# Performance work log

Measured on AMD Instinct MI355X. Metric: run time of the kernel, lower is better.

The kernel has to match this reference:

```python
import jax, jax.numpy as jnp
import numpy as np

B, T, C, H, N = 2, 1024, 2048, 32, 64  # batch, seq, n_embd==dim_att, heads, head_size
EPS_GN = 64e-5  # torch GroupNorm eps=0.00064


def setup_inputs() -> dict:
    key = jax.random.key(0)
    ks = jax.random.split(key, 40)
    def rn(i, shape, s):
        return jax.random.normal(ks[i], shape, dtype=jnp.float32) * s
    return {
        'x': jax.random.normal(ks[0], (B, T, C), dtype=jnp.float32),
        'shift_state': jnp.zeros((B, C), jnp.float32),
        'wkv_state': jnp.zeros((B, H, N, N), jnp.float32),
        'time_maa_x': rn(1, (1, 1, C), 0.3),
        'time_maa_rg': rn(2, (1, 1, C), 0.3),
        'time_maa_wa': rn(3, (1, 1, C), 0.3),
        'time_maa_k': rn(4, (1, 1, C), 0.3),
        'time_maa_v': rn(5, (1, 1, C), 0.3),
        'time_maa_w1': rn(6, (C, 128), 0.02),   # D_MIX_LORA*4 = 128
        'time_maa_w2': rn(7, (4, 32, C), 0.02),
        'time_decay': rn(8, (1, 1, C), 0.5) - 4.0,
        'time_decay_w1': rn(9, (C, 64), 0.02),
        'time_decay_w2': rn(10, (64, C), 0.02),
        'time_faaaa': rn(11, (1, 1, H, N), 0.02),
        'time_aaaaa': rn(12, (1, 1, C), 0.02),
        'time_aaa_w1': rn(13, (C, 16), 0.02),
        'time_aaa_w2': rn(14, (16, C), 0.02),
        'time_kkk_w1': rn(15, (C, 16), 0.02),
        'time_kkk_w2': rn(16, (16, C), 0.02),
        'gate_w1': rn(17, (C, 128), 0.02),
        'gate_w2': rn(18, (128, C), 0.02),
        'ma_w1': rn(19, (C, 16), 0.02),
        'ma_w2': rn(20, (16, C), 0.02),
        'time_misc_a': rn(21, (1, 1, C), 0.02),
        'mk_w1': rn(22, (C, 16), 0.02),
        'mk_w2': rn(23, (16, C), 0.02),
        'time_misc_k': rn(24, (1, 1, C), 0.02),
        'Wr': rn(25, (C, C), 0.5 / np.sqrt(C)),
        'Wk': rn(26, (C, C), 0.05 / np.sqrt(C)),
        'Wv': rn(27, (C, C), 0.5 / np.sqrt(C)),
        'Wo': rn(28, (C, C), 0.5 / np.sqrt(C)),
        'ln_w': jnp.ones((C,), jnp.float32),
        'ln_b': jnp.zeros((C,), jnp.float32),
    }


def _forward(x, shift_state, wkv_state, time_maa_x, time_maa_rg, time_maa_wa,
             time_maa_k, time_maa_v, time_maa_w1, time_maa_w2, time_decay,
             time_decay_w1, time_decay_w2, time_faaaa, time_aaaaa, time_aaa_w1,
             time_aaa_w2, time_kkk_w1, time_kkk_w2, gate_w1, gate_w2, ma_w1,
             ma_w2, time_misc_a, mk_w1, mk_w2, time_misc_k, Wr, Wk, Wv, Wo,
             ln_w, ln_b):
    # token shift difference
    xx = jnp.concatenate([shift_state[:, None, :], x[:, :-1]], axis=1) - x
    xmx = x + xx * time_maa_x
    m = jnp.tanh(xmx @ time_maa_w1).reshape(B, T, 4, -1)   # [B,T,4,32]
    m = jnp.einsum('btfd,fdc->fbtc', m, time_maa_w2)       # [4,B,T,C]
    mrg, mwa, mkm, mv = m[0], m[1], m[2], m[3]
    xrg = x + xx * (time_maa_rg + mrg)
    xwa = x + xx * (time_maa_wa + mwa)
    xk = x + xx * (time_maa_k + mkm)
    xv = x + xx * (time_maa_v + mv)
    r = xrg @ Wr.T
    w = -jax.nn.softplus(-(time_decay + jnp.tanh(xwa @ time_decay_w1) @ time_decay_w2)) - 0.5
    k = xk @ Wk.T
    v = xv @ Wv.T
    g = jnp.tanh(xrg @ gate_w1) @ gate_w2
    kk = k + jnp.tanh(xk @ time_kkk_w1) @ time_kkk_w2
    kkh = kk.reshape(B, T, H, N)
    nrm = jnp.maximum(jnp.linalg.norm(kkh, axis=-1, keepdims=True), 1e-12)  # F.normalize
    kk = (kkh / nrm).reshape(B, T, C)
    a = jax.nn.sigmoid(time_aaaaa + xwa @ time_aaa_w1 @ time_aaa_w2)
    ma = jax.nn.sigmoid(time_misc_a + xwa @ ma_w1 @ ma_w2)
    k = k * ma + k * a * (1.0 - ma)
    mk = jax.nn.sigmoid(time_misc_k + xk @ mk_w1 @ mk_w2)
    k = k * jnp.exp(jnp.minimum(w * mk, 0.0))  # clamp(w*mk, max=0).exp()

    # RWKV-7 recurrence (fused_recurrent_rwkv7 with a=-kk, b=kk*a_gate):
    #   S_t = diag(exp(w_t)) S_{t-1} + b_t (a_t^T S_{t-1}) + k_t v_t^T,  o_t = S_t^T r_t
    def heads(t):
        return jnp.moveaxis(t.reshape(B, T, H, N), 1, 0)  # [T,B,H,N]
    rs, ksq, vs, ws = heads(r), heads(k), heads(v), heads(w)
    a_s, b_s = heads(-kk), heads(kk * a)

    def step(S, inputs):  # S: [B,H,N_key,N_val]
        r_t, k_t, v_t, w_t, a_t, b_t = inputs
        sa = jnp.einsum('bhk,bhkv->bhv', a_t, S)
        S = S * jnp.exp(w_t)[..., None] + k_t[..., None] * v_t[..., None, :] + b_t[..., None] * sa[..., None, :]
        o = jnp.einsum('bhk,bhkv->bhv', r_t, S)
        return S, o

    S_final, o = jax.lax.scan(step, wkv_state, (rs, ksq, vs, ws, a_s, b_s))
    out = jnp.moveaxis(o, 0, 1).reshape(B, T, C)

    # GroupNorm(n_head groups, eps=64e-5), biased variance per head
    y = out.reshape(B * T, H, N)
    mu = y.mean(-1, keepdims=True)
    var = ((y - mu) ** 2).mean(-1, keepdims=True)
    y = (y - mu) / jnp.sqrt(var + EPS_GN)
    y = y * ln_w.reshape(H, N) + ln_b.reshape(H, N)
    xo = y.reshape(B, T, C)

    rh = r.reshape(B, T, H, N)
    kh = k.reshape(B, T, H, N)
    vh = v.reshape(B, T, H, N)
    xo = xo + ((rh * kh * time_faaaa).sum(-1, keepdims=True) * vh).reshape(B, T, C)
    xo = (xo * g) @ Wo.T
    return xo, x[:, -1], S_final


def reference(x, shift_state, wkv_state, time_maa_x, time_maa_rg, time_maa_wa,
              time_maa_k, time_maa_v, time_maa_w1, time_maa_w2, time_decay,
              time_decay_w1, time_decay_w2, time_faaaa, time_aaaaa, time_aaa_w1,
              time_aaa_w2, time_kkk_w1, time_kkk_w2, gate_w1, gate_w2, ma_w1,
              ma_w2, time_misc_a, mk_w1, mk_w2, time_misc_k, Wr, Wk, Wv, Wo,
              ln_w, ln_b):
    return _forward(x, shift_state, wkv_state, time_maa_x, time_maa_rg, time_maa_wa,
                    time_maa_k, time_maa_v, time_maa_w1, time_maa_w2, time_decay,
                    time_decay_w1, time_decay_w2, time_faaaa, time_aaaaa, time_aaa_w1,
                    time_aaa_w2, time_kkk_w1, time_kkk_w2, gate_w1, gate_w2, ma_w1,
                    ma_w2, time_misc_a, mk_w1, mk_w2, time_misc_k, Wr, Wk, Wv, Wo,
                    ln_w, ln_b)
```

## Files before the change

kernel.cpp:

```cpp
#include <hip/hip_runtime.h>
#include <hip/hip_bf16.h>
#include <math.h>


#define B_ 2
#define T_ 1024
#define C_ 2048
#define H_ 32
#define BT_ (B_*T_)
#define BTC_ ((size_t)BT_*C_)
#define CC_ ((size_t)C_*C_)
#define KS_ 8

typedef __bf16 bf16x8 __attribute__((ext_vector_type(8)));
typedef float f32x4 __attribute__((ext_vector_type(4)));

__device__ __forceinline__ float wave64_sum(float v){
#pragma unroll
  for (int d = 1; d < 64; d <<= 1) v += __shfl_xor(v, d, 64);
  return v;
}

__device__ __forceinline__ float dpp_add_xor1(float x){
  int j = __builtin_amdgcn_mov_dpp(__float_as_int(x), 0xB1, 0xF, 0xF, true);
  return x + __int_as_float(j);
}
__device__ __forceinline__ float dpp_add_xor2(float x){
  int j = __builtin_amdgcn_mov_dpp(__float_as_int(x), 0x4E, 0xF, 0xF, true);
  return x + __int_as_float(j);
}
__device__ __forceinline__ float dpp_add_hmir(float x){
  int j = __builtin_amdgcn_mov_dpp(__float_as_int(x), 0x141, 0xF, 0xF, true);
  return x + __int_as_float(j);
}
__device__ __forceinline__ float dpp_add_mir(float x){
  int j = __builtin_amdgcn_mov_dpp(__float_as_int(x), 0x140, 0xF, 0xF, true);
  return x + __int_as_float(j);
}

__device__ __forceinline__ float red16(float x){
  x = dpp_add_xor1(x);
  x = dpp_add_xor2(x);
  x = dpp_add_hmir(x);
  x = dpp_add_mir(x);
  return x;
}

__device__ __forceinline__ size_t bhtn_idx(int r, int c){
  return (((size_t)(r >> 10)*H_ + (c >> 6))*T_ + (r & 1023))*64 + (c & 63);
}

__device__ __forceinline__ void gload_lds16b(const __hip_bfloat16* g, __bf16* l){
  __builtin_amdgcn_global_load_lds((const __attribute__((address_space(1))) void*)g,
                                   (__attribute__((address_space(3))) void*)l, 16, 0, 0);
}

__global__ __launch_bounds__(256) void f2bf_kernel(const float* __restrict__ in,
                                                   __hip_bfloat16* __restrict__ out, size_t n){
  size_t i = (size_t)blockIdx.x*256 + threadIdx.x;
  if (i < n) out[i] = __float2bfloat16(in[i]);
}

__global__ __launch_bounds__(256) void f2bf3_kernel(const float* __restrict__ i0, const float* __restrict__ i1,
                                                    const float* __restrict__ i2,
                                                    __hip_bfloat16* __restrict__ o0, __hip_bfloat16* __restrict__ o1,
                                                    __hip_bfloat16* __restrict__ o2){
  const int z = blockIdx.y;
  const float* in = (z == 0) ? i0 : (z == 1) ? i1 : i2;
  __hip_bfloat16* out = (z == 0) ? o0 : (z == 1) ? o1 : o2;
  size_t i = (size_t)blockIdx.x*256 + threadIdx.x;
  if (i < CC_) out[i] = __float2bfloat16(in[i]);
}

__global__ __launch_bounds__(256) void shift_kernel(const float* __restrict__ x,
                                                    const float* __restrict__ shift,
                                                    const float* __restrict__ maa_x,
                                                    float* __restrict__ xx, __hip_bfloat16* __restrict__ xmx_h,
                                                    float* __restrict__ out1){
  size_t idx = (size_t)blockIdx.x*256 + threadIdx.x;
  int c = (int)(idx % C_);
  size_t bt = idx / C_;
  int t = (int)(bt % T_);
  int b = (int)(bt / T_);
  float xv = x[idx];
  float prev = (t == 0) ? shift[(size_t)b*C_ + c] : x[idx - C_];
  float d = prev - xv;
  xx[idx] = d;
  xmx_h[idx] = __float2bfloat16(xv + d * maa_x[c]);
  if (t == T_-1) out1[(size_t)b*C_ + c] = xv;
}

__global__ __launch_bounds__(256) void tp_pack7(
    const float* __restrict__ w0, const float* __restrict__ w1, const float* __restrict__ w2,
    const float* __restrict__ w3, const float* __restrict__ w4, const float* __restrict__ w5,
    const float* __restrict__ w6, __hip_bfloat16* __restrict__ WtB)
{
  __shared__ float tile[32][33];
  int y = blockIdx.y;
  const float* in; int Nsrc, row_off, panel, yb;
  if      (y < 4)  { in = w0; Nsrc = 128; row_off = 0;  panel = 0; yb = y; }
  else if (y < 6)  { in = w1; Nsrc = 64;  row_off = 0;  panel = 1; yb = y - 4; }
  else if (y < 7)  { in = w2; Nsrc = 16;  row_off = 64; panel = 1; yb = 0; }
  else if (y < 8)  { in = w3; Nsrc = 16;  row_off = 80; panel = 1; yb = 0; }
  else if (y < 12) { in = w4; Nsrc = 128; row_off = 0;  panel = 2; yb = y - 8; }
  else if (y < 13) { in = w5; Nsrc = 16;  row_off = 0;  panel = 3; yb = 0; }
  else             { in = w6; Nsrc = 16;  row_off = 16; panel = 3; yb = 0; }
  __hip_bfloat16* out = WtB + (size_t)panel*128*2048;
  const int t = threadIdx.x;
  const int k0 = blockIdx.x*32, n0 = yb*32;
  const int tn = t & 31, tk = t >> 5;
#pragma unroll
  for (int q = 0; q < 4; q++){
    int ki = tk + 8*q;
    float v = (n0 + tn < Nsrc) ? in[(size_t)(k0+ki)*Nsrc + n0 + tn] : 0.f;
    tile[tn][ki] = v;
  }
  __syncthreads();
#pragma unroll
  for (int q = 0; q < 4; q++){
    int no = tk + 8*q;
    if (n0 + no < Nsrc)
      out[(size_t)(row_off + n0 + no)*2048 + k0 + tn] = __float2bfloat16(tile[no][tn]);
  }
}

__global__ __launch_bounds__(256) void gemm_sk(const __hip_bfloat16* __restrict__ Ah,
                                               const __hip_bfloat16* __restrict__ Bh,
                                               float* __restrict__ parts, int K, int KC){
  __shared__ __bf16 As[2][128*32];
  __shared__ __bf16 Bs[2][128*32];
  const int tid = threadIdx.x;
  const int bm = blockIdx.x*128;
  const int z = blockIdx.y;
  const int wid = tid >> 6, lane = tid & 63;
  const int wr = (wid >> 1)*64, wc = (wid & 1)*64;
  const int fr = lane & 15, kg = lane >> 4;
  const int srow = tid >> 2, sk = (tid & 3)*8;
  f32x4 acc[4][4] = {};
  const int kend = z*KC + KC;
#define SK_STAGE(kt_, b_) do{ \
    gload_lds16b(Ah + (size_t)(bm+srow)*K + (kt_) + sk,    As[b_] + wid*512); \
    gload_lds16b(Ah + (size_t)(bm+srow+64)*K + (kt_) + sk, As[b_] + wid*512 + 64*32); \
    gload_lds16b(Bh + (size_t)(srow)*K + (kt_) + sk,       Bs[b_] + wid*512); \
    gload_lds16b(Bh + (size_t)(srow+64)*K + (kt_) + sk,    Bs[b_] + wid*512 + 64*32); \
  }while(0)
  SK_STAGE(z*KC, 0);
  __builtin_amdgcn_s_waitcnt(0x3F70);
  __builtin_amdgcn_s_barrier();
  __builtin_amdgcn_sched_barrier(0);
  int buf = 0;
  for (int kt = z*KC; kt < kend; kt += 32){
    if (kt + 32 < kend) SK_STAGE(kt+32, buf^1);
    bf16x8 af[4], bfr[4];
#pragma unroll
    for (int i = 0; i < 4; i++){
      af[i]  = *(const bf16x8*)(As[buf] + (wr + i*16 + fr)*32 + kg*8);
      bfr[i] = *(const bf16x8*)(Bs[buf] + (wc + i*16 + fr)*32 + kg*8);
    }
#pragma unroll
    for (int mi = 0; mi < 4; mi++)
#pragma unroll
      for (int ni = 0; ni < 4; ni++)
        acc[mi][ni] = __builtin_amdgcn_mfma_f32_16x16x32_bf16(af[mi], bfr[ni], acc[mi][ni], 0, 0, 0);
    __builtin_amdgcn_sched_barrier(0);
    __builtin_amdgcn_s_waitcnt(0x3F70);
    __builtin_amdgcn_s_barrier();
    __builtin_amdgcn_sched_barrier(0);
    buf ^= 1;
  }
#undef SK_STAGE
  float* Cc = parts + (size_t)z*BT_*128;
  const int orow0 = bm + wr + kg*4;
  const int ocol0 = wc + fr;
#pragma unroll
  for (int mi = 0; mi < 4; mi++)
#pragma unroll
    for (int ni = 0; ni < 4; ni++)
#pragma unroll
      for (int j = 0; j < 4; j++)
        Cc[(size_t)(orow0 + mi*16 + j)*128 + ocol0 + ni*16] = acc[mi][ni][j];
}

__global__ __launch_bounds__(256) void gemm_sk3(
    const __hip_bfloat16* __restrict__ A0, const __hip_bfloat16* __restrict__ A1,
    const __hip_bfloat16* __restrict__ A2,
    const __hip_bfloat16* __restrict__ B0, const __hip_bfloat16* __restrict__ B1,
    const __hip_bfloat16* __restrict__ B2,
    float* __restrict__ P0, float* __restrict__ P1, float* __restrict__ P2, int K, int KC)
{
  __shared__ __bf16 As[2][128*32];
  __shared__ __bf16 Bs[2][128*32];
  const int zi = blockIdx.z;
  const __hip_bfloat16* Ah = (zi == 0) ? A0 : (zi == 1) ? A1 : A2;
  const __hip_bfloat16* Bh = (zi == 0) ? B0 : (zi == 1) ? B1 : B2;
  float* parts = (zi == 0) ? P0 : (zi == 1) ? P1 : P2;
  const int tid = threadIdx.x;
  const int bm = blockIdx.x*128;
  const int z = blockIdx.y;
  const int wid = tid >> 6, lane = tid & 63;
  const int wr = (wid >> 1)*64, wc = (wid & 1)*64;
  const int fr = lane & 15, kg = lane >> 4;
  const int srow = tid >> 2, sk = (tid & 3)*8;
  f32x4 acc[4][4] = {};
  const int kend = z*KC + KC;
#define SK3_STAGE(kt_, b_) do{ \
    gload_lds16b(Ah + (size_t)(bm+srow)*K + (kt_) + sk,    As[b_] + wid*512); \
    gload_lds16b(Ah + (size_t)(bm+srow+64)*K + (kt_) + sk, As[b_] + wid*512 + 64*32); \
    gload_lds16b(Bh + (size_t)(srow)*K + (kt_) + sk,       Bs[b_] + wid*512); \
    gload_lds16b(Bh + (size_t)(srow+64)*K + (kt_) + sk,    Bs[b_] + wid*512 + 64*32); \
  }while(0)
  SK3_STAGE(z*KC, 0);
  __builtin_amdgcn_s_waitcnt(0x3F70);
  __builtin_amdgcn_s_barrier();
  __builtin_amdgcn_sched_barrier(0);
  int buf = 0;
  for (int kt = z*KC; kt < kend; kt += 32){
    if (kt + 32 < kend) SK3_STAGE(kt+32, buf^1);
    bf16x8 af[4], bfr[4];
#pragma unroll
    for (int i = 0; i < 4; i++){
      af[i]  = *(const bf16x8*)(As[buf] + (wr + i*16 + fr)*32 + kg*8);
      bfr[i] = *(const bf16x8*)(Bs[buf] + (wc + i*16 + fr)*32 + kg*8);
    }
#pragma unroll
    for (int mi = 0; mi < 4; mi++)
#pragma unroll
      for (int ni = 0; ni < 4; ni++)
        acc[mi][ni] = __builtin_amdgcn_mfma_f32_16x16x32_bf16(af[mi], bfr[ni], acc[mi][ni], 0, 0, 0);
    __builtin_amdgcn_sched_barrier(0);
    __builtin_amdgcn_s_waitcnt(0x3F70);
    __builtin_amdgcn_s_barrier();
    __builtin_amdgcn_sched_barrier(0);
    buf ^= 1;
  }
#undef SK3_STAGE
  float* Cc = parts + (size_t)z*BT_*128;
  const int orow0 = bm + wr + kg*4;
  const int ocol0 = wc + fr;
#pragma unroll
  for (int mi = 0; mi < 4; mi++)
#pragma unroll
    for (int ni = 0; ni < 4; ni++)
#pragma unroll
      for (int j = 0; j < 4; j++)
        Cc[(size_t)(orow0 + mi*16 + j)*128 + ocol0 + ni*16] = acc[mi][ni][j];
}

__global__ __launch_bounds__(256) void reduce_sk3(const float* __restrict__ P0, const float* __restrict__ P1,
                                                  const float* __restrict__ P2,
                                                  float* __restrict__ O0, float* __restrict__ O1,
                                                  float* __restrict__ O2){
  const int zi = blockIdx.y;
  const float* parts = (zi == 0) ? P0 : (zi == 1) ? P1 : P2;
  float* out = (zi == 0) ? O0 : (zi == 1) ? O1 : O2;
  const int hi = (zi == 0) ? 64 : (zi == 1) ? 128 : 16;
  size_t idx = (size_t)blockIdx.x*256 + threadIdx.x;
  float s = 0.f;
#pragma unroll
  for (int z = 0; z < KS_; z++) s += parts[(size_t)z*BT_*128 + idx];
  int c = (int)(idx & 127);
  if (c < hi) s = tanhf(s);
  out[idx] = s;
}

__global__ __launch_bounds__(256) void reduce_sk(const float* __restrict__ parts, float* __restrict__ out,
                                                 int tanh_lo, int tanh_hi){
  size_t idx = (size_t)blockIdx.x*256 + threadIdx.x;
  float s = 0.f;
#pragma unroll
  for (int z = 0; z < KS_; z++) s += parts[(size_t)z*BT_*128 + idx];
  int c = (int)(idx & 127);
  if (c >= tanh_lo && c < tanh_hi) s = tanhf(s);
  out[idx] = s;
}

__global__ __launch_bounds__(256) void mm_sk_g(const float* __restrict__ A, const float* __restrict__ W,
                                               __hip_bfloat16* __restrict__ out, int K){
  const int j = blockIdx.y*256 + threadIdx.x;
  const int i0 = blockIdx.x*8;
  float acc[8] = {0,0,0,0,0,0,0,0};
  for (int k = 0; k < K; k++){
    float wv = W[(size_t)k*C_ + j];
#pragma unroll
    for (int r = 0; r < 8; r++) acc[r] += A[(size_t)(i0+r)*K + k] * wv;
  }
#pragma unroll
  for (int r = 0; r < 8; r++) out[(size_t)(i0+r)*C_ + j] = __float2bfloat16(acc[r]);
}

__global__ __launch_bounds__(256) void mix_kernel(
    const float* __restrict__ m1, const float* __restrict__ w2,
    const float* __restrict__ x, const float* __restrict__ xx,
    const float* __restrict__ maa_rg, const float* __restrict__ maa_wa,
    const float* __restrict__ maa_k, const float* __restrict__ maa_v,
    __hip_bfloat16* __restrict__ xrg_h, __hip_bfloat16* __restrict__ xwa_h,
    __hip_bfloat16* __restrict__ xk_h, __hip_bfloat16* __restrict__ xv_h)
{
  const int j = blockIdx.y*256 + threadIdx.x;
  const int i0 = blockIdx.x*8;
  float acc[4][8] = {};
#pragma unroll
  for (int f = 0; f < 4; f++){
    for (int d = 0; d < 32; d++){
      float wv = w2[((size_t)f*32 + d)*C_ + j];
#pragma unroll
      for (int r = 0; r < 8; r++)
        acc[f][r] += m1[(size_t)(i0+r)*128 + f*32 + d] * wv;
    }
  }
  float mrg_ = maa_rg[j], mwa_ = maa_wa[j], mk_ = maa_k[j], mv_ = maa_v[j];
#pragma unroll
  for (int r = 0; r < 8; r++){
    size_t idx = (size_t)(i0+r)*C_ + j;
    float xval = x[idx], xxv = xx[idx];
    xrg_h[idx] = __float2bfloat16(xval + xxv*(mrg_ + acc[0][r]));
    xwa_h[idx] = __float2bfloat16(xval + xxv*(mwa_ + acc[1][r]));
    xk_h[idx]  = __float2bfloat16(xval + xxv*(mk_  + acc[2][r]));
    xv_h[idx]  = __float2bfloat16(xval + xxv*(mv_  + acc[3][r]));
  }
}

__global__ __launch_bounds__(256) void gemm_bt(const __hip_bfloat16* __restrict__ Ah,
                                               const __hip_bfloat16* __restrict__ Bh,
                                               float* __restrict__ Cc, int M, int Nn, int K){
  __shared__ __bf16 As[2][128*32];
  __shared__ __bf16 Bs[2][128*32];
  const int tid = threadIdx.x;
  const int bm = blockIdx.x*128, bn = blockIdx.y*128;
  const int wid = tid >> 6, lane = tid & 63;
  const int wr = (wid >> 1)*64, wc = (wid & 1)*64;
  const int fr = lane & 15, kg = lane >> 4;
  const int srow = tid >> 2, sk = (tid & 3)*8;
  f32x4 acc[4][4] = {};
#define BT_STAGE(kt_, b_) do{ \
    gload_lds16b(Ah + (size_t)(bm+srow)*K + (kt_) + sk,    As[b_] + wid*512); \
    gload_lds16b(Ah + (size_t)(bm+srow+64)*K + (kt_) + sk, As[b_] + wid*512 + 64*32); \
    gload_lds16b(Bh + (size_t)(bn+srow)*K + (kt_) + sk,    Bs[b_] + wid*512); \
    gload_lds16b(Bh + (size_t)(bn+srow+64)*K + (kt_) + sk, Bs[b_] + wid*512 + 64*32); \
  }while(0)
  BT_STAGE(0, 0);
  __builtin_amdgcn_s_waitcnt(0x3F70);
  __builtin_amdgcn_s_barrier();
  __builtin_amdgcn_sched_barrier(0);
  int buf = 0;
  for (int kt = 0; kt < K; kt += 32){
    if (kt + 32 < K) BT_STAGE(kt+32, buf^1);
    bf16x8 af[4], bfr[4];
#pragma unroll
    for (int i = 0; i < 4; i++){
      af[i]  = *(const bf16x8*)(As[buf] + (wr + i*16 + fr)*32 + kg*8);
      bfr[i] = *(const bf16x8*)(Bs[buf] + (wc + i*16 + fr)*32 + kg*8);
    }
#pragma unroll
    for (int mi = 0; mi < 4; mi++)
#pragma unroll
      for (int ni = 0; ni < 4; ni++)
        acc[mi][ni] = __builtin_amdgcn_mfma_f32_16x16x32_bf16(af[mi], bfr[ni], acc[mi][ni], 0, 0, 0);
    __builtin_amdgcn_sched_barrier(0);
    __builtin_amdgcn_s_waitcnt(0x3F70);
    __builtin_amdgcn_s_barrier();
    __builtin_amdgcn_sched_barrier(0);
    buf ^= 1;
  }
#undef BT_STAGE
  const int orow0 = bm + wr + kg*4;
  const int ocol0 = bn + wc + fr;
#pragma unroll
  for (int mi = 0; mi < 4; mi++)
#pragma unroll
    for (int ni = 0; ni < 4; ni++)
#pragma unroll
      for (int j = 0; j < 4; j++)
        Cc[(size_t)(orow0 + mi*16 + j)*Nn + ocol0 + ni*16] = acc[mi][ni][j];
}

__global__ __launch_bounds__(256) void gemm_bt_T3(
    const __hip_bfloat16* __restrict__ A0, const __hip_bfloat16* __restrict__ A1,
    const __hip_bfloat16* __restrict__ A2,
    const __hip_bfloat16* __restrict__ B0, const __hip_bfloat16* __restrict__ B1,
    const __hip_bfloat16* __restrict__ B2,
    float* __restrict__ C0, float* __restrict__ C1, float* __restrict__ C2, int K)
{
  __shared__ __bf16 As[2][128*32];
  __shared__ __bf16 Bs[2][128*32];
  const int zi = blockIdx.z;
  const __hip_bfloat16* Ah = (zi == 0) ? A0 : (zi == 1) ? A1 : A2;
  const __hip_bfloat16* Bh = (zi == 0) ? B0 : (zi == 1) ? B1 : B2;
  float* Cc = (zi == 0) ? C0 : (zi == 1) ? C1 : C2;
  const int tid = threadIdx.x;
  const int bm = blockIdx.x*128, bn = blockIdx.y*128;
  const int wid = tid >> 6, lane = tid & 63;
  const int wr = (wid >> 1)*64, wc = (wid & 1)*64;
  const int fr = lane & 15, kg = lane >> 4;
  const int srow = tid >> 2, sk = (tid & 3)*8;
  f32x4 acc[4][4] = {};
#define T3_STAGE(kt_, b_) do{ \
    gload_lds16b(Ah + (size_t)(bm+srow)*K + (kt_) + sk,    As[b_] + wid*512); \
    gload_lds16b(Ah + (size_t)(bm+srow+64)*K + (kt_) + sk, As[b_] + wid*512 + 64*32); \
    gload_lds16b(Bh + (size_t)(bn+srow)*K + (kt_) + sk,    Bs[b_] + wid*512); \
    gload_lds16b(Bh + (size_t)(bn+srow+64)*K + (kt_) + sk, Bs[b_] + wid*512 + 64*32); \
  }while(0)
  T3_STAGE(0, 0);
  __builtin_amdgcn_s_waitcnt(0x3F70);
  __builtin_amdgcn_s_barrier();
  __builtin_amdgcn_sched_barrier(0);
  int buf = 0;
  for (int kt = 0; kt < K; kt += 32){
    if (kt + 32 < K) T3_STAGE(kt+32, buf^1);
    bf16x8 af[4], bfr[4];
#pragma unroll
    for (int i = 0; i < 4; i++){
      af[i]  = *(const bf16x8*)(As[buf] + (wr + i*16 + fr)*32 + kg*8);
      bfr[i] = *(const bf16x8*)(Bs[buf] + (wc + i*16 + fr)*32 + kg*8);
    }
#pragma unroll
    for (int mi = 0; mi < 4; mi++)
#pragma unroll
      for (int ni = 0; ni < 4; ni++)
        acc[mi][ni] = __builtin_amdgcn_mfma_f32_16x16x32_bf16(af[mi], bfr[ni], acc[mi][ni], 0, 0, 0);
    __builtin_amdgcn_sched_barrier(0);
    __builtin_amdgcn_s_waitcnt(0x3F70);
    __builtin_amdgcn_s_barrier();
    __builtin_amdgcn_sched_barrier(0);
    buf ^= 1;
  }
#undef T3_STAGE
  const int r0 = bm + wr + kg*4;
  const int c0 = bn + wc + fr;
#pragma unroll
  for (int mi = 0; mi < 4; mi++)
#pragma unroll
    for (int ni = 0; ni < 4; ni++)
#pragma unroll
      for (int j = 0; j < 4; j++)
        Cc[bhtn_idx(r0 + mi*16 + j, c0 + ni*16)] = acc[mi][ni][j];
}

__global__ __launch_bounds__(256) void lora2_kernel(
    const float* __restrict__ wa1, const float* __restrict__ k1c,
    const float* __restrict__ dw2, const float* __restrict__ aw2, const float* __restrict__ maw2,
    const float* __restrict__ mkw2, const float* __restrict__ kkw2,
    const float* __restrict__ td, const float* __restrict__ aaaaa,
    const float* __restrict__ misc_a, const float* __restrict__ misc_k,
    float* __restrict__ k0, float* __restrict__ b_out,
    float* __restrict__ ew_out, float* __restrict__ kk0_out)
{
  const int j = blockIdx.y*256 + threadIdx.x;
  const int i0 = blockIdx.x*8;
  float accW[8] = {}, accA[8] = {}, accMA[8] = {}, accMK[8] = {}, accKK[8] = {};
  for (int k = 0; k < 64; k++){
    float wv = dw2[(size_t)k*C_ + j];
#pragma unroll
    for (int r = 0; r < 8; r++) accW[r] += wa1[(size_t)(i0+r)*128 + k] * wv;
  }
  for (int k = 0; k < 16; k++){
    float w_a  = aw2[(size_t)k*C_ + j];
    float w_ma = maw2[(size_t)k*C_ + j];
    float w_mk = mkw2[(size_t)k*C_ + j];
    float w_kk = kkw2[(size_t)k*C_ + j];
#pragma unroll
    for (int r = 0; r < 8; r++){
      accA[r]  += wa1[(size_t)(i0+r)*128 + 64 + k] * w_a;
      accMA[r] += wa1[(size_t)(i0+r)*128 + 80 + k] * w_ma;
      accKK[r] += k1c[(size_t)(i0+r)*128 + k] * w_kk;
      accMK[r] += k1c[(size_t)(i0+r)*128 + 16 + k] * w_mk;
    }
  }
  float tdv = td[j], aav = aaaaa[j], mav = misc_a[j], mkv = misc_k[j];
#pragma unroll
  for (int r = 0; r < 8; r++){
    size_t idx = bhtn_idx(i0+r, j);
    float u  = tdv + accW[r];
    float w  = -log1pf(expf(-u)) - 0.5f;
    float a  = 1.f/(1.f + expf(-(aav + accA[r])));
    float ma = 1.f/(1.f + expf(-(mav + accMA[r])));
    float mk = 1.f/(1.f + expf(-(mkv + accMK[r])));
    float kv = k0[idx];
    float kk = kv + accKK[r];
    float ss  = wave64_sum(kk*kk);
    float kkn = kk / fmaxf(sqrtf(ss), 1e-12f);
    kk0_out[idx] = kkn;
    b_out[idx]   = kkn * a;
    float kn = kv * (ma + a*(1.f - ma)) * expf(fminf(w*mk, 0.f));
    k0[idx] = kn;
    ew_out[idx] = expf(w);
  }
}

__global__ __launch_bounds__(64, 1) void rec_kernel(
    const float* __restrict__ rr, const float* __restrict__ kx,
    const float* __restrict__ vx, const float* __restrict__ ew,
    const float* __restrict__ kkv, const float* __restrict__ bsv,
    const float* __restrict__ s0, float* __restrict__ o, float* __restrict__ sT)
{
  const int g = blockIdx.x;
  const int bh = g & 63;
  const int vg = g >> 6;
  const int b = bh >> 5, h = bh & 31;
  const int lane = threadIdx.x;
  const int cf = lane >> 4;
  const int kq = lane & 15;
  const int k0 = kq*4;
  const int v = vg*4 + cf;

  float S0, S1, S2, S3;
  {
    const float* p = s0 + ((size_t)bh*64 + k0)*64 + v;
    S0 = p[0]; S1 = p[64]; S2 = p[128]; S3 = p[192];
  }

  const size_t sb = (size_t)bh*T_*64;
  const float* gA = kkv + sb + k0;
  const float* gE = ew  + sb + k0;
  const float* gK = kx  + sb + k0;
  const float* gB = bsv + sb + k0;
  const float* gR = rr  + sb + k0;
  const float* gV = vx  + sb + v;
  float* ob = o + (size_t)b*T_*C_ + h*64 + v;

  float4 Aq[8], Eq[8], Kq[8], Bq[8], Rq[8];
  float  Vq[8];

#define LOADT(t_, sl_) do{ \
    Aq[sl_] = *(const float4*)(gA + (size_t)(t_)*64); \
    Eq[sl_] = *(const float4*)(gE + (size_t)(t_)*64); \
    Kq[sl_] = *(const float4*)(gK + (size_t)(t_)*64); \
    Bq[sl_] = *(const float4*)(gB + (size_t)(t_)*64); \
    Rq[sl_] = *(const float4*)(gR + (size_t)(t_)*64); \
    Vq[sl_] = gV[(size_t)(t_)*64]; \
  }while(0)

  LOADT(0, 0); LOADT(1, 1); LOADT(2, 2); LOADT(3, 3);
  LOADT(4, 4); LOADT(5, 5); LOADT(6, 6);

  for (int tb = 0; tb < T_; tb += 8){
#pragma unroll
    for (int s = 0; s < 8; s++){
      const int t = tb + s;
      const int tn = (t + 7 < T_) ? (t + 7) : (T_ - 1);
      LOADT(tn, (s + 7) & 7);
      const float4 A  = Aq[s];
      const float4 E  = Eq[s];
      const float4 Kk = Kq[s];
      const float4 Bv = Bq[s];
      const float4 R  = Rq[s];
      const float  vt = Vq[s];
      float p = (A.x*S0 + A.y*S1) + (A.z*S2 + A.w*S3);
      p = red16(p);
      S0 = S0*E.x + Kk.x*vt - Bv.x*p;
      S1 = S1*E.y + Kk.y*vt - Bv.y*p;
      S2 = S2*E.z + Kk.z*vt - Bv.z*p;
      S3 = S3*E.w + Kk.w*vt - Bv.w*p;
      float op = (R.x*S0 + R.y*S1) + (R.z*S2 + R.w*S3);
      op = red16(op);
      if (kq == 0)
        ob[(size_t)t*C_] = op;
    }
  }
#undef LOADT
  float* pT = sT + ((size_t)bh*64 + k0)*64 + v;
  pT[0] = S0; pT[64] = S1; pT[128] = S2; pT[192] = S3;
}

__global__ __launch_bounds__(256) void post_kernel(
    const float* __restrict__ o, const float* __restrict__ r, const float* __restrict__ k,
    const float* __restrict__ v, const __hip_bfloat16* __restrict__ g,
    const float* __restrict__ lnw, const float* __restrict__ lnb,
    const float* __restrict__ faaaa, __hip_bfloat16* __restrict__ z_h)
{
  const size_t grp = (size_t)blockIdx.x*4 + (threadIdx.x >> 6);
  const int lane = threadIdx.x & 63;
  const int h = (int)(grp & (H_-1));
  const int bt = (int)(grp >> 5);
  const size_t idx  = grp*64 + lane;
  const size_t idx2 = (((size_t)(bt >> 10)*H_ + h)*T_ + (bt & 1023))*64 + lane;
  const int ci = h*64 + lane;
  float y = o[idx];
  float mu = wave64_sum(y) * (1.f/64.f);
  float d = y - mu;
  float var = wave64_sum(d*d) * (1.f/64.f);
  float yn = d * rsqrtf(var + 64e-5f) * lnw[ci] + lnb[ci];
  float s = wave64_sum(r[idx2]*k[idx2]*faaaa[ci]);
  float xo = yn + s*v[idx2];
  z_h[idx] = __float2bfloat16(xo * __bfloat162float(g[idx]));
}

extern "C" void kernel_launch(void* const* d_in, const int* in_sizes, int n_in,
                              void* d_out, int out_size, void* d_ws, size_t ws_size,
                              hipStream_t stream){
  (void)in_sizes; (void)n_in; (void)out_size;
  const float* x      = (const float*)d_in[0];
  const float* shift  = (const float*)d_in[1];
  const float* wkv0   = (const float*)d_in[2];
  const float* maa_x  = (const float*)d_in[3];
  const float* maa_rg = (const float*)d_in[4];
  const float* maa_wa = (const float*)d_in[5];
  const float* maa_k  = (const float*)d_in[6];
  const float* maa_v  = (const float*)d_in[7];
  const float* maa_w1 = (const float*)d_in[8];
  const float* maa_w2 = (const float*)d_in[9];
  const float* tdecay = (const float*)d_in[10];
  const float* dw1    = (const float*)d_in[11];
  const float* dw2    = (const float*)d_in[12];
  const float* faaaa  = (const float*)d_in[13];
  const float* aaaaa  = (const float*)d_in[14];
  const float* aw1    = (const float*)d_in[15];
  const float* aw2    = (const float*)d_in[16];
  const float* kkw1   = (const float*)d_in[17];
  const float* kkw2   = (const float*)d_in[18];
  const float* gw1    = (const float*)d_in[19];
  const float* gw2    = (const float*)d_in[20];
  const float* maw1   = (const float*)d_in[21];
  const float* maw2   = (const float*)d_in[22];
  const float* misc_a = (const float*)d_in[23];
  const float* mkw1   = (const float*)d_in[24];
  const float* mkw2   = (const float*)d_in[25];
  const float* misc_k = (const float*)d_in[26];
  const float* Wr     = (const float*)d_in[27];
  const float* Wk     = (const float*)d_in[28];
  const float* Wv     = (const float*)d_in[29];
  const float* Wo     = (const float*)d_in[30];
  const float* lnw    = (const float*)d_in[31];
  const float* lnb    = (const float*)d_in[32];

  float* out0 = (float*)d_out;
  float* out1 = out0 + BTC_;
  float* outS = out1 + (size_t)B_*C_;

  const size_t NEEDED = (6*BTC_ + (size_t)3*BT_*128)*4 + 5*CC_*2 + (size_t)4*128*2048*2;
  if (ws_size < NEEDED) return;

  float* ws = (float*)d_ws;
  float* rbuf  = ws;
  float* kbuf  = ws + 1*BTC_;
  float* vbuf  = ws + 2*BTC_;
  float* abuf  = ws + 3*BTC_;
  float* ewbuf = ws + 4*BTC_;
  float* kkbuf = ws + 5*BTC_;
  float* xx    = abuf;
  float* wa1   = ws + 6*BTC_;
  float* g1f   = wa1 + (size_t)BT_*128;
  float* k1c   = g1f + (size_t)BT_*128;
  float* parts = rbuf;
  float* m1f   = vbuf;
  __hip_bfloat16* hb = (__hip_bfloat16*)(k1c + (size_t)BT_*128);
  __hip_bfloat16* xrg_h = hb;
  __hip_bfloat16* xwa_h = hb + 1*CC_;
  __hip_bfloat16* xk_h  = hb + 2*CC_;
  __hip_bfloat16* xv_h  = hb + 3*CC_;
  __hip_bfloat16* Wb    = hb + 4*CC_;
  __hip_bfloat16* WtB   = hb + 5*CC_;
  __hip_bfloat16* Wt_m  = WtB;
  __hip_bfloat16* Wt_wa = WtB + (size_t)128*2048;
  __hip_bfloat16* Wt_g  = WtB + (size_t)2*128*2048;
  __hip_bfloat16* Wt_k  = WtB + (size_t)3*128*2048;
  __hip_bfloat16* xmx_h = xv_h;
  __hip_bfloat16* g_h   = xwa_h;
  __hip_bfloat16* z_h   = xv_h;
  __hip_bfloat16* Wk_h  = (__hip_bfloat16*)ewbuf;
  __hip_bfloat16* Wv_h  = (__hip_bfloat16*)kkbuf;

  dim3 blk(256);
  const int KC = C_/KS_;

  hipMemsetAsync(WtB, 0, (size_t)4*128*2048*2, stream);
  tp_pack7<<<dim3(64, 14), blk, 0, stream>>>(maa_w1, dw1, aw1, maw1, gw1, kkw1, mkw1, WtB);

  shift_kernel<<<(int)(BTC_/256), blk, 0, stream>>>(x, shift, maa_x, xx, xmx_h, out1);

  gemm_sk<<<dim3(BT_/128, KS_), blk, 0, stream>>>(xmx_h, Wt_m, parts, C_, KC);
  reduce_sk<<<BT_*128/256, blk, 0, stream>>>(parts, m1f, 0, 128);

  mix_kernel<<<dim3(BT_/8, C_/256), blk, 0, stream>>>(m1f, maa_w2, x, xx, maa_rg, maa_wa, maa_k, maa_v,
                                                      xrg_h, xwa_h, xk_h, xv_h);

  gemm_sk3<<<dim3(BT_/128, KS_, 3), blk, 0, stream>>>(xwa_h, xrg_h, xk_h,
                                                      Wt_wa, Wt_g, Wt_k,
                                                      rbuf, kbuf, vbuf, C_, KC);
  reduce_sk3<<<dim3(BT_*128/256, 3), blk, 0, stream>>>(rbuf, kbuf, vbuf, wa1, g1f, k1c);

  mm_sk_g<<<dim3(BT_/8, C_/256), blk, 0, stream>>>(g1f, gw2, g_h, 128);

  f2bf3_kernel<<<dim3((int)(CC_/256), 3), blk, 0, stream>>>(Wr, Wk, Wv, Wb, Wk_h, Wv_h);
  gemm_bt_T3<<<dim3(BT_/128, C_/128, 3), blk, 0, stream>>>(xrg_h, xk_h, xv_h,
                                                           Wb, Wk_h, Wv_h,
                                                           rbuf, kbuf, vbuf, C_);

  lora2_kernel<<<dim3(BT_/8, C_/256), blk, 0, stream>>>(wa1, k1c,
                                                        dw2, aw2, maw2, mkw2, kkw2,
                                                        tdecay, aaaaa, misc_a, misc_k,
                                                        kbuf, abuf, ewbuf, kkbuf);

  rec_kernel<<<1024, dim3(64), 0, stream>>>(rbuf, kbuf, vbuf, ewbuf, kkbuf, abuf, wkv0, out0, outS);

  post_kernel<<<BT_*H_/4, blk, 0, stream>>>(out0, rbuf, kbuf, vbuf, g_h, lnw, lnb, faaaa, z_h);
  f2bf_kernel<<<(int)(CC_/256), blk, 0, stream>>>(Wo, Wb, CC_);
  gemm_bt<<<dim3(BT_/128, C_/128), blk, 0, stream>>>(z_h, Wb, out0, BT_, C_, C_);
}
```

Measured before the change: 704.3 us.

## Triple-buffer LDS tiles in all bf16 MFMA GEMM kernels

Converts the double-buffered LDS pipelines in the split-K and full GEMM kernels to a three-stage ring, issuing two tile loads ahead. The waitcnt now lets one load group stay outstanding instead of draining all loads each iteration, so global-to-LDS latency can overlap more compute. LDS use per block grows from 32KB to 48KB, which may lower occupancy. The code also assumes at least two K tiles per block.

```diff
diff --git a/kernel.cpp b/kernel.cpp
--- a/kernel.cpp
+++ b/kernel.cpp
@@ -127,8 +127,8 @@
 __global__ __launch_bounds__(256) void gemm_sk(const __hip_bfloat16* __restrict__ Ah,
                                                const __hip_bfloat16* __restrict__ Bh,
                                                float* __restrict__ parts, int K, int KC){
-  __shared__ __bf16 As[2][128*32];
-  __shared__ __bf16 Bs[2][128*32];
+  __shared__ __bf16 As[3][128*32];
+  __shared__ __bf16 Bs[3][128*32];
   const int tid = threadIdx.x;
   const int bm = blockIdx.x*128;
   const int z = blockIdx.y;
@@ -137,38 +137,52 @@
   const int fr = lane & 15, kg = lane >> 4;
   const int srow = tid >> 2, sk = (tid & 3)*8;
   f32x4 acc[4][4] = {};
-  const int kend = z*KC + KC;
+  const int kb = z*KC;
+  const int NT = KC >> 5;
 #define SK_STAGE(kt_, b_) do{ \
     gload_lds16b(Ah + (size_t)(bm+srow)*K + (kt_) + sk,    As[b_] + wid*512); \
     gload_lds16b(Ah + (size_t)(bm+srow+64)*K + (kt_) + sk, As[b_] + wid*512 + 64*32); \
     gload_lds16b(Bh + (size_t)(srow)*K + (kt_) + sk,       Bs[b_] + wid*512); \
     gload_lds16b(Bh + (size_t)(srow+64)*K + (kt_) + sk,    Bs[b_] + wid*512 + 64*32); \
   }while(0)
-  SK_STAGE(z*KC, 0);
+#define SK_COMPUTE(b_) do{ \
+    bf16x8 af[4], bfr[4]; \
+    _Pragma("unroll") \
+    for (int i = 0; i < 4; i++){ \
+      af[i]  = *(const bf16x8*)(As[b_] + (wr + i*16 + fr)*32 + kg*8); \
+      bfr[i] = *(const bf16x8*)(Bs[b_] + (wc + i*16 + fr)*32 + kg*8); \
+    } \
+    _Pragma("unroll") \
+    for (int mi = 0; mi < 4; mi++) \
+      _Pragma("unroll") \
+      for (int ni = 0; ni < 4; ni++) \
+        acc[mi][ni] = __builtin_amdgcn_mfma_f32_16x16x32_bf16(af[mi], bfr[ni], acc[mi][ni], 0, 0, 0); \
+  }while(0)
+  SK_STAGE(kb, 0);
+  SK_STAGE(kb + 32, 1);
+  __builtin_amdgcn_s_waitcnt(0x3F74);
+  __builtin_amdgcn_s_barrier();
+  __builtin_amdgcn_sched_barrier(0);
+  int cur = 0;
+  for (int t = 0; t < NT-2; ++t){
+    int nx = cur + 2; if (nx >= 3) nx -= 3;
+    SK_STAGE(kb + (t+2)*32, nx);
+    SK_COMPUTE(cur);
+    __builtin_amdgcn_sched_barrier(0);
+    __builtin_amdgcn_s_waitcnt(0x3F74);
+    __builtin_amdgcn_s_barrier();
+    __builtin_amdgcn_sched_barrier(0);
+    cur = (cur+1 == 3) ? 0 : cur+1;
+  }
+  SK_COMPUTE(cur);
+  __builtin_amdgcn_sched_barrier(0);
   __builtin_amdgcn_s_waitcnt(0x3F70);
   __builtin_amdgcn_s_barrier();
   __builtin_amdgcn_sched_barrier(0);
-  int buf = 0;
-  for (int kt = z*KC; kt < kend; kt += 32){
-    if (kt + 32 < kend) SK_STAGE(kt+32, buf^1);
-    bf16x8 af[4], bfr[4];
-#pragma unroll
-    for (int i = 0; i < 4; i++){
-      af[i]  = *(const bf16x8*)(As[buf] + (wr + i*16 + fr)*32 + kg*8);
-      bfr[i] = *(const bf16x8*)(Bs[buf] + (wc + i*16 + fr)*32 + kg*8);
-    }
-#pragma unroll
-    for (int mi = 0; mi < 4; mi++)
-#pragma unroll
-      for (int ni = 0; ni < 4; ni++)
-        acc[mi][ni] = __builtin_amdgcn_mfma_f32_16x16x32_bf16(af[mi], bfr[ni], acc[mi][ni], 0, 0, 0);
-    __builtin_amdgcn_sched_barrier(0);
-    __builtin_amdgcn_s_waitcnt(0x3F70);
-    __builtin_amdgcn_s_barrier();
-    __builtin_amdgcn_sched_barrier(0);
-    buf ^= 1;
-  }
+  cur = (cur+1 == 3) ? 0 : cur+1;
+  SK_COMPUTE(cur);
 #undef SK_STAGE
+#undef SK_COMPUTE
   float* Cc = parts + (size_t)z*BT_*128;
   const int orow0 = bm + wr + kg*4;
   const int ocol0 = wc + fr;
@@ -188,8 +202,8 @@
     const __hip_bfloat16* __restrict__ B2,
     float* __restrict__ P0, float* __restrict__ P1, float* __restrict__ P2, int K, int KC)
 {
-  __shared__ __bf16 As[2][128*32];
-  __shared__ __bf16 Bs[2][128*32];
+  __shared__ __bf16 As[3][128*32];
+  __shared__ __bf16 Bs[3][128*32];
   const int zi = blockIdx.z;
   const __hip_bfloat16* Ah = (zi == 0) ? A0 : (zi == 1) ? A1 : A2;
   const __hip_bfloat16* Bh = (zi == 0) ? B0 : (zi == 1) ? B1 : B2;
@@ -202,38 +216,52 @@
   const int fr = lane & 15, kg = lane >> 4;
   const int srow = tid >> 2, sk = (tid & 3)*8;
   f32x4 acc[4][4] = {};
-  const int kend = z*KC + KC;
+  const int kb = z*KC;
+  const int NT = KC >> 5;
 #define SK3_STAGE(kt_, b_) do{ \
     gload_lds16b(Ah + (size_t)(bm+srow)*K + (kt_) + sk,    As[b_] + wid*512); \
     gload_lds16b(Ah + (size_t)(bm+srow+64)*K + (kt_) + sk, As[b_] + wid*512 + 64*32); \
     gload_lds16b(Bh + (size_t)(srow)*K + (kt_) + sk,       Bs[b_] + wid*512); \
     gload_lds16b(Bh + (size_t)(srow+64)*K + (kt_) + sk,    Bs[b_] + wid*512 + 64*32); \
   }while(0)
-  SK3_STAGE(z*KC, 0);
+#define SK3_COMPUTE(b_) do{ \
+    bf16x8 af[4], bfr[4]; \
+    _Pragma("unroll") \
+    for (int i = 0; i < 4; i++){ \
+      af[i]  = *(const bf16x8*)(As[b_] + (wr + i*16 + fr)*32 + kg*8); \
+      bfr[i] = *(const bf16x8*)(Bs[b_] + (wc + i*16 + fr)*32 + kg*8); \
+    } \
+    _Pragma("unroll") \
+    for (int mi = 0; mi < 4; mi++) \
+      _Pragma("unroll") \
+      for (int ni = 0; ni < 4; ni++) \
+        acc[mi][ni] = __builtin_amdgcn_mfma_f32_16x16x32_bf16(af[mi], bfr[ni], acc[mi][ni], 0, 0, 0); \
+  }while(0)
+  SK3_STAGE(kb, 0);
+  SK3_STAGE(kb + 32, 1);
+  __builtin_amdgcn_s_waitcnt(0x3F74);
+  __builtin_amdgcn_s_barrier();
+  __builtin_amdgcn_sched_barrier(0);
+  int cur = 0;
+  for (int t = 0; t < NT-2; ++t){
+    int nx = cur + 2; if (nx >= 3) nx -= 3;
+    SK3_STAGE(kb + (t+2)*32, nx);
+    SK3_COMPUTE(cur);
+    __builtin_amdgcn_sched_barrier(0);
+    __builtin_amdgcn_s_waitcnt(0x3F74);
+    __builtin_amdgcn_s_barrier();
+    __builtin_amdgcn_sched_barrier(0);
+    cur = (cur+1 == 3) ? 0 : cur+1;
+  }
+  SK3_COMPUTE(cur);
+  __builtin_amdgcn_sched_barrier(0);
   __builtin_amdgcn_s_waitcnt(0x3F70);
   __builtin_amdgcn_s_barrier();
   __builtin_amdgcn_sched_barrier(0);
-  int buf = 0;
-  for (int kt = z*KC; kt < kend; kt += 32){
-    if (kt + 32 < kend) SK3_STAGE(kt+32, buf^1);
-    bf16x8 af[4], bfr[4];
-#pragma unroll
-    for (int i = 0; i < 4; i++){
-      af[i]  = *(const bf16x8*)(As[buf] + (wr + i*16 + fr)*32 + kg*8);
-      bfr[i] = *(const bf16x8*)(Bs[buf] + (wc + i*16 + fr)*32 + kg*8);
-    }
-#pragma unroll
-    for (int mi = 0; mi < 4; mi++)
-#pragma unroll
-      for (int ni = 0; ni < 4; ni++)
-        acc[mi][ni] = __builtin_amdgcn_mfma_f32_16x16x32_bf16(af[mi], bfr[ni], acc[mi][ni], 0, 0, 0);
-    __builtin_amdgcn_sched_barrier(0);
-    __builtin_amdgcn_s_waitcnt(0x3F70);
-    __builtin_amdgcn_s_barrier();
-    __builtin_amdgcn_sched_barrier(0);
-    buf ^= 1;
-  }
+  cur = (cur+1 == 3) ? 0 : cur+1;
+  SK3_COMPUTE(cur);
 #undef SK3_STAGE
+#undef SK3_COMPUTE
   float* Cc = parts + (size_t)z*BT_*128;
   const int orow0 = bm + wr + kg*4;
   const int ocol0 = wc + fr;
@@ -323,8 +351,8 @@
 __global__ __launch_bounds__(256) void gemm_bt(const __hip_bfloat16* __restrict__ Ah,
                                                const __hip_bfloat16* __restrict__ Bh,
                                                float* __restrict__ Cc, int M, int Nn, int K){
-  __shared__ __bf16 As[2][128*32];
-  __shared__ __bf16 Bs[2][128*32];
+  __shared__ __bf16 As[3][128*32];
+  __shared__ __bf16 Bs[3][128*32];
   const int tid = threadIdx.x;
   const int bm = blockIdx.x*128, bn = blockIdx.y*128;
   const int wid = tid >> 6, lane = tid & 63;
@@ -332,37 +360,51 @@
   const int fr = lane & 15, kg = lane >> 4;
   const int srow = tid >> 2, sk = (tid & 3)*8;
   f32x4 acc[4][4] = {};
+  const int NT = K >> 5;
 #define BT_STAGE(kt_, b_) do{ \
     gload_lds16b(Ah + (size_t)(bm+srow)*K + (kt_) + sk,    As[b_] + wid*512); \
     gload_lds16b(Ah + (size_t)(bm+srow+64)*K + (kt_) + sk, As[b_] + wid*512 + 64*32); \
     gload_lds16b(Bh + (size_t)(bn+srow)*K + (kt_) + sk,    Bs[b_] + wid*512); \
     gload_lds16b(Bh + (size_t)(bn+srow+64)*K + (kt_) + sk, Bs[b_] + wid*512 + 64*32); \
   }while(0)
+#define BT_COMPUTE(b_) do{ \
+    bf16x8 af[4], bfr[4]; \
+    _Pragma("unroll") \
+    for (int i = 0; i < 4; i++){ \
+      af[i]  = *(const bf16x8*)(As[b_] + (wr + i*16 + fr)*32 + kg*8); \
+      bfr[i] = *(const bf16x8*)(Bs[b_] + (wc + i*16 + fr)*32 + kg*8); \
+    } \
+    _Pragma("unroll") \
+    for (int mi = 0; mi < 4; mi++) \
+      _Pragma("unroll") \
+      for (int ni = 0; ni < 4; ni++) \
+        acc[mi][ni] = __builtin_amdgcn_mfma_f32_16x16x32_bf16(af[mi], bfr[ni], acc[mi][ni], 0, 0, 0); \
+  }while(0)
   BT_STAGE(0, 0);
+  BT_STAGE(32, 1);
+  __builtin_amdgcn_s_waitcnt(0x3F74);
+  __builtin_amdgcn_s_barrier();
+  __builtin_amdgcn_sched_barrier(0);
+  int cur = 0;
+  for (int t = 0; t < NT-2; ++t){
+    int nx = cur + 2; if (nx >= 3) nx -= 3;
+    BT_STAGE((t+2)*32, nx);
+    BT_COMPUTE(cur);
+    __builtin_amdgcn_sched_barrier(0);
+    __builtin_amdgcn_s_waitcnt(0x3F74);
+    __builtin_amdgcn_s_barrier();
+    __builtin_amdgcn_sched_barrier(0);
+    cur = (cur+1 == 3) ? 0 : cur+1;
+  }
+  BT_COMPUTE(cur);
+  __builtin_amdgcn_sched_barrier(0);
   __builtin_amdgcn_s_waitcnt(0x3F70);
   __builtin_amdgcn_s_barrier();
   __builtin_amdgcn_sched_barrier(0);
-  int buf = 0;
-  for (int kt = 0; kt < K; kt += 32){
-    if (kt + 32 < K) BT_STAGE(kt+32, buf^1);
-    bf16x8 af[4], bfr[4];
-#pragma unroll
-    for (int i = 0; i < 4; i++){
-      af[i]  = *(const bf16x8*)(As[buf] + (wr + i*16 + fr)*32 + kg*8);
-      bfr[i] = *(const bf16x8*)(Bs[buf] + (wc + i*16 + fr)*32 + kg*8);
-    }
-#pragma unroll
-    for (int mi = 0; mi < 4; mi++)
-#pragma unroll
-      for (int ni = 0; ni < 4; ni++)
-        acc[mi][ni] = __builtin_amdgcn_mfma_f32_16x16x32_bf16(af[mi], bfr[ni], acc[mi][ni], 0, 0, 0);
-    __builtin_amdgcn_sched_barrier(0);
-    __builtin_amdgcn_s_waitcnt(0x3F70);
-    __builtin_amdgcn_s_barrier();
-    __builtin_amdgcn_sched_barrier(0);
-    buf ^= 1;
-  }
+  cur = (cur+1 == 3) ? 0 : cur+1;
+  BT_COMPUTE(cur);
 #undef BT_STAGE
+#undef BT_COMPUTE
   const int orow0 = bm + wr + kg*4;
   const int ocol0 = bn + wc + fr;
 #pragma unroll
@@ -381,8 +423,8 @@
     const __hip_bfloat16* __restrict__ B2,
     float* __restrict__ C0, float* __restrict__ C1, float* __restrict__ C2, int K)
 {
-  __shared__ __bf16 As[2][128*32];
-  __shared__ __bf16 Bs[2][128*32];
+  __shared__ __bf16 As[3][128*32];
+  __shared__ __bf16 Bs[3][128*32];
   const int zi = blockIdx.z;
   const __hip_bfloat16* Ah = (zi == 0) ? A0 : (zi == 1) ? A1 : A2;
   const __hip_bfloat16* Bh = (zi == 0) ? B0 : (zi == 1) ? B1 : B2;
@@ -394,37 +436,51 @@
   const int fr = lane & 15, kg = lane >> 4;
   const int srow = tid >> 2, sk = (tid & 3)*8;
   f32x4 acc[4][4] = {};
+  const int NT = K >> 5;
 #define T3_STAGE(kt_, b_) do{ \
     gload_lds16b(Ah + (size_t)(bm+srow)*K + (kt_) + sk,    As[b_] + wid*512); \
     gload_lds16b(Ah + (size_t)(bm+srow+64)*K + (kt_) + sk, As[b_] + wid*512 + 64*32); \
     gload_lds16b(Bh + (size_t)(bn+srow)*K + (kt_) + sk,    Bs[b_] + wid*512); \
     gload_lds16b(Bh + (size_t)(bn+srow+64)*K + (kt_) + sk, Bs[b_] + wid*512 + 64*32); \
   }while(0)
+#define T3_COMPUTE(b_) do{ \
+    bf16x8 af[4], bfr[4]; \
+    _Pragma("unroll") \
+    for (int i = 0; i < 4; i++){ \
+      af[i]  = *(const bf16x8*)(As[b_] + (wr + i*16 + fr)*32 + kg*8); \
+      bfr[i] = *(const bf16x8*)(Bs[b_] + (wc + i*16 + fr)*32 + kg*8); \
+    } \
+    _Pragma("unroll") \
+    for (int mi = 0; mi < 4; mi++) \
+      _Pragma("unroll") \
+      for (int ni = 0; ni < 4; ni++) \
+        acc[mi][ni] = __builtin_amdgcn_mfma_f32_16x16x32_bf16(af[mi], bfr[ni], acc[mi][ni], 0, 0, 0); \
+  }while(0)
   T3_STAGE(0, 0);
+  T3_STAGE(32, 1);
+  __builtin_amdgcn_s_waitcnt(0x3F74);
+  __builtin_amdgcn_s_barrier();
+  __builtin_amdgcn_sched_barrier(0);
+  int cur = 0;
+  for (int t = 0; t < NT-2; ++t){
+    int nx = cur + 2; if (nx >= 3) nx -= 3;
+    T3_STAGE((t+2)*32, nx);
+    T3_COMPUTE(cur);
+    __builtin_amdgcn_sched_barrier(0);
+    __builtin_amdgcn_s_waitcnt(0x3F74);
+    __builtin_amdgcn_s_barrier();
+    __builtin_amdgcn_sched_barrier(0);
+    cur = (cur+1 == 3) ? 0 : cur+1;
+  }
+  T3_COMPUTE(cur);
+  __builtin_amdgcn_sched_barrier(0);
   __builtin_amdgcn_s_waitcnt(0x3F70);
   __builtin_amdgcn_s_barrier();
   __builtin_amdgcn_sched_barrier(0);
-  int buf = 0;
-  for (int kt = 0; kt < K; kt += 32){
-    if (kt + 32 < K) T3_STAGE(kt+32, buf^1);
-    bf16x8 af[4], bfr[4];
-#pragma unroll
-    for (int i = 0; i < 4; i++){
-      af[i]  = *(const bf16x8*)(As[buf] + (wr + i*16 + fr)*32 + kg*8);
-      bfr[i] = *(const bf16x8*)(Bs[buf] + (wc + i*16 + fr)*32 + kg*8);
-    }
-#pragma unroll
-    for (int mi = 0; mi < 4; mi++)
-#pragma unroll
-      for (int ni = 0; ni < 4; ni++)
-        acc[mi][ni] = __builtin_amdgcn_mfma_f32_16x16x32_bf16(af[mi], bfr[ni], acc[mi][ni], 0, 0, 0);
-    __builtin_amdgcn_sched_barrier(0);
-    __builtin_amdgcn_s_waitcnt(0x3F70);
-    __builtin_amdgcn_s_barrier();
-    __builtin_amdgcn_sched_barrier(0);
-    buf ^= 1;
-  }
+  cur = (cur+1 == 3) ? 0 : cur+1;
+  T3_COMPUTE(cur);
 #undef T3_STAGE
+#undef T3_COMPUTE
   const int r0 = bm + wr + kg*4;
   const int c0 = bn + wc + fr;
 #pragma unroll
```

Result: no change. 705.7 us (+0.2%).
